# Optimization experiments

Measured on AMD Instinct MI355X. Metric: run time of the kernel, lower is better.

## Reference

```python
import jax, jax.numpy as jnp
import numpy as np

N = 100000   # nodes
E = 1600000  # edges (avg degree 16)
F_IN = 256
H = 64
C = 16


def setup_inputs() -> dict:
    key = jax.random.key(0)
    k1, k2, k3, k4 = jax.random.split(key, 4)
    x = jax.random.normal(k1, (N, F_IN), jnp.float32)
    edge_index = jax.random.randint(k2, (2, E), 0, N, jnp.int32)
    W1 = jax.random.normal(k3, (F_IN, H), jnp.float32) * (1.0 / np.sqrt(F_IN))
    b1 = jnp.zeros((H,), jnp.float32)
    W2 = jax.random.normal(k4, (H, C), jnp.float32) * (1.0 / np.sqrt(H))
    b2 = jnp.zeros((C,), jnp.float32)
    return {"x": x, "edge_index": edge_index, "W1": W1, "b1": b1, "W2": W2, "b2": b2}


def _gcn_conv(h_in, src, dst, norm, W, b):
    # linear transform first (GCNConv: lin has no bias), then normalized scatter-add
    h = h_in @ W                                  # [N, out]
    msg = jnp.take(h, src, axis=0) * norm[:, None]  # [E+N, out] gathered + scaled
    out = jax.ops.segment_sum(msg, dst, num_segments=h_in.shape[0])
    return out + b


def reference(x, edge_index, W1, b1, W2, b2):
    num_nodes = x.shape[0]
    # add self-loops (GCNConv default, edge_weight = 1)
    loop = jnp.arange(num_nodes, dtype=edge_index.dtype)
    src = jnp.concatenate([edge_index[0], loop])
    dst = jnp.concatenate([edge_index[1], loop])
    # symmetric normalization D^{-1/2} A D^{-1/2}
    deg = jax.ops.segment_sum(jnp.ones_like(dst, dtype=x.dtype), dst, num_segments=num_nodes)
    dinv = jnp.where(deg > 0, jax.lax.rsqrt(deg), 0.0)
    norm = jnp.take(dinv, src) * jnp.take(dinv, dst)  # [E+N]
    h = jax.nn.relu(_gcn_conv(x, src, dst, norm, W1, b1))
    # dropout is identity in eval mode
    out = _gcn_conv(h, src, dst, norm, W2, b2)
    return jax.nn.log_softmax(out, axis=1)
```

## Files before the change

kernel.cpp:

```cpp
#include <hip/hip_runtime.h>
#include <hip/hip_fp16.h>
#include <math.h>

#define N_NODES 100000
#define N_EDGES 1600000
#define FIN 256
#define NB 196
#define CAP 10240

typedef _Float16 h8 __attribute__((ext_vector_type(8)));
typedef float f4 __attribute__((ext_vector_type(4)));

__global__ __launch_bounds__(256) void k_prepW1(const float* __restrict__ W1, _Float16* __restrict__ Bfrag) {
    int i = blockIdx.x * 256 + threadIdx.x;
    int j = i & 7, lane = (i >> 3) & 63, nt = (i >> 9) & 3, ks = i >> 11;
    int k = ks * 32 + ((lane >> 4) << 3) + j;
    int c = nt * 16 + (lane & 15);
    Bfrag[i] = (_Float16)W1[k * 64 + c];
}

__global__ __launch_bounds__(256) void k_fill_bins(const int* __restrict__ src, const int* __restrict__ dst,
                                                   int* __restrict__ bcur, int* __restrict__ bpack) {
    __shared__ int hist[NB], curs[NB], bstart[NB];
    const int tid = threadIdx.x;
    for (int i = tid; i < NB; i += 256) { hist[i] = 0; curs[i] = 0; }
    __syncthreads();
    const int base = blockIdx.x * 4096;
    int eb[16], ee[16];
    #pragma unroll
    for (int k = 0; k < 16; ++k) {
        int e = base + k * 256 + tid;
        eb[k] = -1;
        if (e < N_EDGES) {
            int s = src[e], d = dst[e];
            int b = d >> 9;
            eb[k] = b;
            ee[k] = ((d & 511) << 17) | s;
            atomicAdd(&hist[b], 1);
        }
    }
    __syncthreads();
    for (int i = tid; i < NB; i += 256)
        if (hist[i] > 0) bstart[i] = i * CAP + atomicAdd(&bcur[i], hist[i]);
    __syncthreads();
    #pragma unroll
    for (int k = 0; k < 16; ++k) {
        if (eb[k] >= 0) {
            int r = atomicAdd(&curs[eb[k]], 1);
            bpack[bstart[eb[k]] + r] = ee[k];
        }
    }
}

__global__ __launch_bounds__(512) void k_sort_bins(const int* __restrict__ bcur,
                                                   const int* __restrict__ bpack,
                                                   int* __restrict__ pack,
                                                   int* __restrict__ starts,
                                                   int* __restrict__ ends,
                                                   float* __restrict__ dinv) {
    __shared__ int hist[512], sd[512], cur[512];
    const int tid = threadIdx.x;
    const int b = blockIdx.x;
    const int node0 = b << 9;
    hist[tid] = 0;
    __syncthreads();
    const int s0 = b * CAP, s1 = s0 + bcur[b];
    for (int i = s0 + tid; i < s1; i += 512) atomicAdd(&hist[bpack[i] >> 17], 1);
    __syncthreads();
    const int deg = hist[tid];
    sd[tid] = deg;
    __syncthreads();
    for (int off = 1; off < 512; off <<= 1) {
        int tv = (tid >= off) ? sd[tid - off] : 0;
        __syncthreads();
        sd[tid] += tv;
        __syncthreads();
    }
    const int excl = sd[tid] - deg;
    const int n = node0 + tid;
    cur[tid] = s0 + excl;
    if (n < N_NODES) {
        starts[n] = s0 + excl;
        ends[n]   = s0 + excl + deg;
        dinv[n] = rsqrtf((float)deg + 1.0f);
    }
    __syncthreads();
    for (int i = s0 + tid; i < s1; i += 512) {
        int v = bpack[i];
        int pos = atomicAdd(&cur[v >> 17], 1);
        pack[pos] = v & 0x1FFFF;
    }
}

__global__ __launch_bounds__(256) void k_gemm1(const float* __restrict__ x,
                                               const _Float16* __restrict__ Bfrag,
                                               const float* __restrict__ dinv,
                                               __half* __restrict__ hh) {
    const int tid = threadIdx.x;
    const int wave = tid >> 6, lane = tid & 63;
    const int lrow = lane & 15;
    const int lk = lane >> 4;
    const int row = blockIdx.x * 64 + wave * 16 + lrow;
    const int rowc = (row < N_NODES) ? row : (N_NODES - 1);
    const float di = dinv[rowc];
    const float* xp = x + (size_t)rowc * 256 + lk * 8;
    const h8* bp = (const h8*)Bfrag + lane;

    f4 acc0 = {0.f, 0.f, 0.f, 0.f};
    f4 acc1 = {0.f, 0.f, 0.f, 0.f};
    f4 acc2 = {0.f, 0.f, 0.f, 0.f};
    f4 acc3 = {0.f, 0.f, 0.f, 0.f};

    #pragma unroll 2
    for (int ks = 0; ks < 8; ++ks) {
        float4 a01 = *(const float4*)(xp + ks * 32);
        float4 a23 = *(const float4*)(xp + ks * 32 + 4);
        h8 af;
        af[0] = (_Float16)(a01.x * di); af[1] = (_Float16)(a01.y * di);
        af[2] = (_Float16)(a01.z * di); af[3] = (_Float16)(a01.w * di);
        af[4] = (_Float16)(a23.x * di); af[5] = (_Float16)(a23.y * di);
        af[6] = (_Float16)(a23.z * di); af[7] = (_Float16)(a23.w * di);
        h8 b0 = bp[(ks * 4 + 0) * 64];
        h8 b1 = bp[(ks * 4 + 1) * 64];
        h8 b2 = bp[(ks * 4 + 2) * 64];
        h8 b3 = bp[(ks * 4 + 3) * 64];
        acc0 = __builtin_amdgcn_mfma_f32_16x16x32_f16(af, b0, acc0, 0, 0, 0);
        acc1 = __builtin_amdgcn_mfma_f32_16x16x32_f16(af, b1, acc1, 0, 0, 0);
        acc2 = __builtin_amdgcn_mfma_f32_16x16x32_f16(af, b2, acc2, 0, 0, 0);
        acc3 = __builtin_amdgcn_mfma_f32_16x16x32_f16(af, b3, acc3, 0, 0, 0);
    }

    const int orow0 = blockIdx.x * 64 + wave * 16 + lk * 4;
    const bool evlane = ((lane & 1) == 0);
#define STORE_TILE(ACC, NT) { \
    _Pragma("unroll") \
    for (int r = 0; r < 4; ++r) { \
        float v = ACC[r]; \
        float o = __shfl_xor(v, 1); \
        int orow = orow0 + r; \
        if (evlane && orow < N_NODES) \
            *(__half2*)&hh[(size_t)orow * 64 + (NT) * 16 + lrow] = __floats2half2_rn(v, o); \
    } }
    STORE_TILE(acc0, 0)
    STORE_TILE(acc1, 1)
    STORE_TILE(acc2, 2)
    STORE_TILE(acc3, 3)
#undef STORE_TILE
}

__global__ __launch_bounds__(256) void k_agg1_gemm2(const int* __restrict__ starts,
                                                    const int* __restrict__ ends,
                                                    const int* __restrict__ pack,
                                                    const float* __restrict__ dinv,
                                                    const __half* __restrict__ hh,
                                                    const float* __restrict__ b1,
                                                    const float* __restrict__ W2,
                                                    __half* __restrict__ h2h) {
    __shared__ float W2s[64][17];
    __shared__ float h1s[4][64];
    const int tid = threadIdx.x;
    for (int i = tid; i < 64 * 16; i += 256) W2s[i >> 4][i & 15] = W2[i];
    __syncthreads();

    const int wave = tid >> 6;
    const int lane = tid & 63;
    const int node = blockIdx.x * 4 + wave;
    const int e4 = lane >> 4;
    const int l4 = lane & 15;

    const int s0 = starts[node], s1 = ends[node];
    float4 A = {0.f, 0.f, 0.f, 0.f}, B = {0.f, 0.f, 0.f, 0.f};
    int i = s0;
    for (; i + 7 < s1; i += 8) {
        int p0 = pack[i + e4], p1 = pack[i + 4 + e4];
        uint2 r0 = *(const uint2*)(hh + (size_t)p0 * 64 + 4 * l4);
        uint2 r1 = *(const uint2*)(hh + (size_t)p1 * 64 + 4 * l4);
        float2 f00 = __half22float2(*(const __half2*)&r0.x);
        float2 f01 = __half22float2(*(const __half2*)&r0.y);
        float2 f10 = __half22float2(*(const __half2*)&r1.x);
        float2 f11 = __half22float2(*(const __half2*)&r1.y);
        A.x += f00.x; A.y += f00.y; A.z += f01.x; A.w += f01.y;
        B.x += f10.x; B.y += f10.y; B.z += f11.x; B.w += f11.y;
    }
    for (; i + 3 < s1; i += 4) {
        int p = pack[i + e4];
        uint2 r = *(const uint2*)(hh + (size_t)p * 64 + 4 * l4);
        float2 f0 = __half22float2(*(const __half2*)&r.x);
        float2 f1 = __half22float2(*(const __half2*)&r.y);
        A.x += f0.x; A.y += f0.y; A.z += f1.x; A.w += f1.y;
    }
    if (i + e4 < s1) {
        int p = pack[i + e4];
        uint2 r = *(const uint2*)(hh + (size_t)p * 64 + 4 * l4);
        float2 f0 = __half22float2(*(const __half2*)&r.x);
        float2 f1 = __half22float2(*(const __half2*)&r.y);
        A.x += f0.x; A.y += f0.y; A.z += f1.x; A.w += f1.y;
    }
    A.x += B.x; A.y += B.y; A.z += B.z; A.w += B.w;
    A.x += __shfl_xor(A.x, 16); A.y += __shfl_xor(A.y, 16);
    A.z += __shfl_xor(A.z, 16); A.w += __shfl_xor(A.w, 16);
    A.x += __shfl_xor(A.x, 32); A.y += __shfl_xor(A.y, 32);
    A.z += __shfl_xor(A.z, 32); A.w += __shfl_xor(A.w, 32);

    const float di = dinv[node];
    if (lane < 16) {
        uint2 sr = *(const uint2*)(hh + (size_t)node * 64 + 4 * l4);
        float2 sf0 = __half22float2(*(const __half2*)&sr.x);
        float2 sf1 = __half22float2(*(const __half2*)&sr.y);
        h1s[wave][4 * l4 + 0] = fmaxf((A.x + sf0.x) * di + b1[4 * l4 + 0], 0.f);
        h1s[wave][4 * l4 + 1] = fmaxf((A.y + sf0.y) * di + b1[4 * l4 + 1], 0.f);
        h1s[wave][4 * l4 + 2] = fmaxf((A.z + sf1.x) * di + b1[4 * l4 + 2], 0.f);
        h1s[wave][4 * l4 + 3] = fmaxf((A.w + sf1.y) * di + b1[4 * l4 + 3], 0.f);
    }
    const int j = lane >> 4, cc = lane & 15;
    float g = 0.f;
    #pragma unroll
    for (int t = 0; t < 16; ++t) {
        int k = j * 16 + t;
        g = fmaf(h1s[wave][k], W2s[k][cc], g);
    }
    g += __shfl_xor(g, 16);
    g += __shfl_xor(g, 32);
    g *= di;
    float go = __shfl_xor(g, 1);
    if (lane < 16 && (cc & 1) == 0) {
        *(__half2*)&h2h[(size_t)node * 16 + cc] = __floats2half2_rn(g, go);
    }
}

__global__ __launch_bounds__(256) void k_agg2_final(const int* __restrict__ starts,
                                                    const int* __restrict__ ends,
                                                    const int* __restrict__ pack,
                                                    const float* __restrict__ dinv,
                                                    const __half* __restrict__ h2h,
                                                    const float* __restrict__ b2,
                                                    float* __restrict__ out) {
    const int tid = threadIdx.x;
    const int wave = tid >> 6;
    const int lane = tid & 63;
    const int node = blockIdx.x * 4 + wave;
    const int j = lane >> 3, cp = lane & 7;

    const int s0 = starts[node], s1 = ends[node];
    float2 a0 = {0.f, 0.f}, a1 = {0.f, 0.f};
    int i = s0 + j;
    for (; i + 8 < s1; i += 16) {
        int p0 = pack[i], p1 = pack[i + 8];
        float2 f0 = __half22float2(*(const __half2*)(h2h + (size_t)p0 * 16 + 2 * cp));
        float2 f1 = __half22float2(*(const __half2*)(h2h + (size_t)p1 * 16 + 2 * cp));
        a0.x += f0.x; a0.y += f0.y;
        a1.x += f1.x; a1.y += f1.y;
    }
    for (; i < s1; i += 8) {
        int p = pack[i];
        float2 f = __half22float2(*(const __half2*)(h2h + (size_t)p * 16 + 2 * cp));
        a0.x += f.x; a0.y += f.y;
    }
    float2 z;
    z.x = a0.x + a1.x;
    z.y = a0.y + a1.y;
    z.x += __shfl_xor(z.x, 8);  z.y += __shfl_xor(z.y, 8);
    z.x += __shfl_xor(z.x, 16); z.y += __shfl_xor(z.y, 16);
    z.x += __shfl_xor(z.x, 32); z.y += __shfl_xor(z.y, 32);

    const float di = dinv[node];
    float2 sf = __half22float2(*(const __half2*)(h2h + (size_t)node * 16 + 2 * cp));
    z.x = (z.x + sf.x) * di + b2[2 * cp];
    z.y = (z.y + sf.y) * di + b2[2 * cp + 1];

    float m = fmaxf(z.x, z.y);
    m = fmaxf(m, __shfl_xor(m, 1, 8));
    m = fmaxf(m, __shfl_xor(m, 2, 8));
    m = fmaxf(m, __shfl_xor(m, 4, 8));
    float ex = __expf(z.x - m), ey = __expf(z.y - m);
    float s = ex + ey;
    s += __shfl_xor(s, 1, 8);
    s += __shfl_xor(s, 2, 8);
    s += __shfl_xor(s, 4, 8);
    float ls = logf(s);
    if (j == 0) {
        float2 o;
        o.x = z.x - m - ls;
        o.y = z.y - m - ls;
        *(float2*)&out[(size_t)node * 16 + 2 * cp] = o;
    }
}

extern "C" void kernel_launch(void* const* d_in, const int* in_sizes, int n_in,
                              void* d_out, int out_size, void* d_ws, size_t ws_size,
                              hipStream_t stream) {
    const float* x  = (const float*)d_in[0];
    const int* ei   = (const int*)d_in[1];
    const float* W1 = (const float*)d_in[2];
    const float* b1 = (const float*)d_in[3];
    const float* W2 = (const float*)d_in[4];
    const float* b2 = (const float*)d_in[5];
    const int* src = ei;
    const int* dst = ei + N_EDGES;

    _Float16* Bfrag = (_Float16*)d_ws;
    int*    bcur    = (int*)d_ws + 8192;
    int*    starts  = bcur + NB;
    int*    ends    = starts + N_NODES;
    float*  dinv    = (float*)(ends + N_NODES);
    int*    bpack   = (int*)(dinv + N_NODES);
    int*    pack    = bpack + NB * CAP;
    __half* hh      = (__half*)(pack + NB * CAP);
    __half* h2h     = hh + (size_t)N_NODES * 64;
    float*  out     = (float*)d_out;

    hipMemsetAsync(bcur, 0, NB * sizeof(int), stream);

    k_prepW1<<<64, 256, 0, stream>>>(W1, Bfrag);
    k_fill_bins<<<(N_EDGES + 4095) / 4096, 256, 0, stream>>>(src, dst, bcur, bpack);
    k_sort_bins<<<NB, 512, 0, stream>>>(bcur, bpack, pack, starts, ends, dinv);
    k_gemm1<<<(N_NODES + 63) / 64, 256, 0, stream>>>(x, Bfrag, dinv, hh);
    k_agg1_gemm2<<<N_NODES / 4, 256, 0, stream>>>(starts, ends, pack, dinv, hh, b1, W2, h2h);
    k_agg2_final<<<N_NODES / 4, 256, 0, stream>>>(starts, ends, pack, dinv, h2h, b2, out);
}
```

Baseline: 181.5 us.

## Split layer-1 features into column quarters for cache-friendly aggregation, separate GEMM2

The layer-1 transformed features are stored as four column-quarter planes of 16 halves each, so each aggregation pass gathers from a 3.2 MB working set that fits better in cache. Aggregation runs as four interleaved block groups, one per quarter, and processes 16 edges per wave step. The fused aggregation+GEMM2 kernel is split into k_agg1q plus a separate k_gemm2 that reads the intermediate h1 back from memory. The split adds a kernel launch and an extra write and read of the hidden activations, and the neighbor index lists are now read four times.

Result: slower. 224.0 us (+23.4%).

```diff
diff --git a/kernel.cpp b/kernel.cpp
--- a/kernel.cpp
+++ b/kernel.cpp
@@ -139,7 +139,7 @@
         float o = __shfl_xor(v, 1); \
         int orow = orow0 + r; \
         if (evlane && orow < N_NODES) \
-            *(__half2*)&hh[(size_t)orow * 64 + (NT) * 16 + lrow] = __floats2half2_rn(v, o); \
+            *(__half2*)&hh[((size_t)(NT) * N_NODES + orow) * 16 + lrow] = __floats2half2_rn(v, o); \
     } }
     STORE_TILE(acc0, 0)
     STORE_TILE(acc1, 1)
@@ -148,84 +148,99 @@
 #undef STORE_TILE
 }
 
-__global__ __launch_bounds__(256) void k_agg1_gemm2(const int* __restrict__ starts,
-                                                    const int* __restrict__ ends,
-                                                    const int* __restrict__ pack,
-                                                    const float* __restrict__ dinv,
-                                                    const __half* __restrict__ hh,
-                                                    const float* __restrict__ b1,
-                                                    const float* __restrict__ W2,
-                                                    __half* __restrict__ h2h) {
+__global__ __launch_bounds__(256) void k_agg1q(const int* __restrict__ starts,
+                                               const int* __restrict__ ends,
+                                               const int* __restrict__ pack,
+                                               const float* __restrict__ dinv,
+                                               const __half* __restrict__ hh,
+                                               const float* __restrict__ b1,
+                                               __half* __restrict__ h1p) {
+    const int tid = threadIdx.x;
+    const int q = blockIdx.x & 3;
+    const int g = blockIdx.x >> 2;
+    const int wave = tid >> 6, lane = tid & 63;
+    const int e16 = lane >> 2, c4 = lane & 3;
+    const __half* hq = hh + (size_t)q * N_NODES * 16;
+
+    for (int nn = 0; nn < 4; ++nn) {
+        const int node = g * 16 + wave * 4 + nn;
+        const int s0 = starts[node], s1 = ends[node];
+        float4 A = {0.f, 0.f, 0.f, 0.f}, Bv = {0.f, 0.f, 0.f, 0.f};
+        int i = s0;
+        for (; i + 31 < s1; i += 32) {
+            int p0 = pack[i + e16], p1 = pack[i + 16 + e16];
+            uint2 r0 = *(const uint2*)(hq + (size_t)p0 * 16 + c4 * 4);
+            uint2 r1 = *(const uint2*)(hq + (size_t)p1 * 16 + c4 * 4);
+            float2 f00 = __half22float2(*(const __half2*)&r0.x);
+            float2 f01 = __half22float2(*(const __half2*)&r0.y);
+            float2 f10 = __half22float2(*(const __half2*)&r1.x);
+            float2 f11 = __half22float2(*(const __half2*)&r1.y);
+            A.x += f00.x; A.y += f00.y; A.z += f01.x; A.w += f01.y;
+            Bv.x += f10.x; Bv.y += f10.y; Bv.z += f11.x; Bv.w += f11.y;
+        }
+        for (; i < s1; i += 16) {
+            if (i + e16 < s1) {
+                int p = pack[i + e16];
+                uint2 r = *(const uint2*)(hq + (size_t)p * 16 + c4 * 4);
+                float2 f0 = __half22float2(*(const __half2*)&r.x);
+                float2 f1 = __half22float2(*(const __half2*)&r.y);
+                A.x += f0.x; A.y += f0.y; A.z += f1.x; A.w += f1.y;
+            }
+        }
+        A.x += Bv.x; A.y += Bv.y; A.z += Bv.z; A.w += Bv.w;
+        A.x += __shfl_xor(A.x, 4);  A.y += __shfl_xor(A.y, 4);
+        A.z += __shfl_xor(A.z, 4);  A.w += __shfl_xor(A.w, 4);
+        A.x += __shfl_xor(A.x, 8);  A.y += __shfl_xor(A.y, 8);
+        A.z += __shfl_xor(A.z, 8);  A.w += __shfl_xor(A.w, 8);
+        A.x += __shfl_xor(A.x, 16); A.y += __shfl_xor(A.y, 16);
+        A.z += __shfl_xor(A.z, 16); A.w += __shfl_xor(A.w, 16);
+        A.x += __shfl_xor(A.x, 32); A.y += __shfl_xor(A.y, 32);
+        A.z += __shfl_xor(A.z, 32); A.w += __shfl_xor(A.w, 32);
+        if (lane < 4) {
+            const float di = dinv[node];
+            uint2 sr = *(const uint2*)(hq + (size_t)node * 16 + c4 * 4);
+            float2 sf0 = __half22float2(*(const __half2*)&sr.x);
+            float2 sf1 = __half22float2(*(const __half2*)&sr.y);
+            const float* bq = b1 + q * 16 + c4 * 4;
+            float v0 = fmaxf((A.x + sf0.x) * di + bq[0], 0.f);
+            float v1 = fmaxf((A.y + sf0.y) * di + bq[1], 0.f);
+            float v2 = fmaxf((A.z + sf1.x) * di + bq[2], 0.f);
+            float v3 = fmaxf((A.w + sf1.y) * di + bq[3], 0.f);
+            __half2 o0 = __floats2half2_rn(v0, v1);
+            __half2 o1 = __floats2half2_rn(v2, v3);
+            uint2 ov = { *(unsigned*)&o0, *(unsigned*)&o1 };
+            *(uint2*)(h1p + ((size_t)q * N_NODES + node) * 16 + c4 * 4) = ov;
+        }
+    }
+}
+
+__global__ __launch_bounds__(256) void k_gemm2(const __half* __restrict__ h1p,
+                                               const float* __restrict__ dinv,
+                                               const float* __restrict__ W2,
+                                               __half* __restrict__ h2h) {
     __shared__ float W2s[64][17];
-    __shared__ float h1s[4][64];
+    __shared__ float h1s[16][65];
     const int tid = threadIdx.x;
     for (int i = tid; i < 64 * 16; i += 256) W2s[i >> 4][i & 15] = W2[i];
-    __syncthreads();
-
-    const int wave = tid >> 6;
-    const int lane = tid & 63;
-    const int node = blockIdx.x * 4 + wave;
-    const int e4 = lane >> 4;
-    const int l4 = lane & 15;
-
-    const int s0 = starts[node], s1 = ends[node];
-    float4 A = {0.f, 0.f, 0.f, 0.f}, B = {0.f, 0.f, 0.f, 0.f};
-    int i = s0;
-    for (; i + 7 < s1; i += 8) {
-        int p0 = pack[i + e4], p1 = pack[i + 4 + e4];
-        uint2 r0 = *(const uint2*)(hh + (size_t)p0 * 64 + 4 * l4);
-        uint2 r1 = *(const uint2*)(hh + (size_t)p1 * 64 + 4 * l4);
-        float2 f00 = __half22float2(*(const __half2*)&r0.x);
-        float2 f01 = __half22float2(*(const __half2*)&r0.y);
-        float2 f10 = __half22float2(*(const __half2*)&r1.x);
-        float2 f11 = __half22float2(*(const __half2*)&r1.y);
-        A.x += f00.x; A.y += f00.y; A.z += f01.x; A.w += f01.y;
-        B.x += f10.x; B.y += f10.y; B.z += f11.x; B.w += f11.y;
-    }
-    for (; i + 3 < s1; i += 4) {
-        int p = pack[i + e4];
-        uint2 r = *(const uint2*)(hh + (size_t)p * 64 + 4 * l4);
+    const int node0 = blockIdx.x * 16;
+    {
+        int n = tid >> 4, c0 = (tid & 15) * 4;
+        int q = c0 >> 4, cin = c0 & 15;
+        uint2 r = *(const uint2*)(h1p + ((size_t)q * N_NODES + node0 + n) * 16 + cin);
         float2 f0 = __half22float2(*(const __half2*)&r.x);
         float2 f1 = __half22float2(*(const __half2*)&r.y);
-        A.x += f0.x; A.y += f0.y; A.z += f1.x; A.w += f1.y;
-    }
-    if (i + e4 < s1) {
-        int p = pack[i + e4];
-        uint2 r = *(const uint2*)(hh + (size_t)p * 64 + 4 * l4);
-        float2 f0 = __half22float2(*(const __half2*)&r.x);
-        float2 f1 = __half22float2(*(const __half2*)&r.y);
-        A.x += f0.x; A.y += f0.y; A.z += f1.x; A.w += f1.y;
-    }
-    A.x += B.x; A.y += B.y; A.z += B.z; A.w += B.w;
-    A.x += __shfl_xor(A.x, 16); A.y += __shfl_xor(A.y, 16);
-    A.z += __shfl_xor(A.z, 16); A.w += __shfl_xor(A.w, 16);
-    A.x += __shfl_xor(A.x, 32); A.y += __shfl_xor(A.y, 32);
-    A.z += __shfl_xor(A.z, 32); A.w += __shfl_xor(A.w, 32);
-
-    const float di = dinv[node];
-    if (lane < 16) {
-        uint2 sr = *(const uint2*)(hh + (size_t)node * 64 + 4 * l4);
-        float2 sf0 = __half22float2(*(const __half2*)&sr.x);
-        float2 sf1 = __half22float2(*(const __half2*)&sr.y);
-        h1s[wave][4 * l4 + 0] = fmaxf((A.x + sf0.x) * di + b1[4 * l4 + 0], 0.f);
-        h1s[wave][4 * l4 + 1] = fmaxf((A.y + sf0.y) * di + b1[4 * l4 + 1], 0.f);
-        h1s[wave][4 * l4 + 2] = fmaxf((A.z + sf1.x) * di + b1[4 * l4 + 2], 0.f);
-        h1s[wave][4 * l4 + 3] = fmaxf((A.w + sf1.y) * di + b1[4 * l4 + 3], 0.f);
-    }
-    const int j = lane >> 4, cc = lane & 15;
+        h1s[n][c0 + 0] = f0.x; h1s[n][c0 + 1] = f0.y;
+        h1s[n][c0 + 2] = f1.x; h1s[n][c0 + 3] = f1.y;
+    }
+    __syncthreads();
+    const int n = tid >> 4, c = tid & 15;
     float g = 0.f;
     #pragma unroll
-    for (int t = 0; t < 16; ++t) {
-        int k = j * 16 + t;
-        g = fmaf(h1s[wave][k], W2s[k][cc], g);
-    }
-    g += __shfl_xor(g, 16);
-    g += __shfl_xor(g, 32);
-    g *= di;
+    for (int k = 0; k < 64; ++k) g = fmaf(h1s[n][k], W2s[k][c], g);
+    g *= dinv[node0 + n];
     float go = __shfl_xor(g, 1);
-    if (lane < 16 && (cc & 1) == 0) {
-        *(__half2*)&h2h[(size_t)node * 16 + cc] = __floats2half2_rn(g, go);
-    }
+    if ((c & 1) == 0)
+        *(__half2*)&h2h[(size_t)(node0 + n) * 16 + c] = __floats2half2_rn(g, go);
 }
 
 __global__ __launch_bounds__(256) void k_agg2_final(const int* __restrict__ starts,
@@ -306,7 +321,8 @@
     int*    bpack   = (int*)(dinv + N_NODES);
     int*    pack    = bpack + NB * CAP;
     __half* hh      = (__half*)(pack + NB * CAP);
-    __half* h2h     = hh + (size_t)N_NODES * 64;
+    __half* h1p     = hh + (size_t)N_NODES * 64;
+    __half* h2h     = h1p + (size_t)N_NODES * 64;
     float*  out     = (float*)d_out;
 
     hipMemsetAsync(bcur, 0, NB * sizeof(int), stream);
@@ -315,6 +331,7 @@
     k_fill_bins<<<(N_EDGES + 4095) / 4096, 256, 0, stream>>>(src, dst, bcur, bpack);
     k_sort_bins<<<NB, 512, 0, stream>>>(bcur, bpack, pack, starts, ends, dinv);
     k_gemm1<<<(N_NODES + 63) / 64, 256, 0, stream>>>(x, Bfrag, dinv, hh);
-    k_agg1_gemm2<<<N_NODES / 4, 256, 0, stream>>>(starts, ends, pack, dinv, hh, b1, W2, h2h);
+    k_agg1q<<<(N_NODES / 16) * 4, 256, 0, stream>>>(starts, ends, pack, dinv, hh, b1, h1p);
+    k_gemm2<<<N_NODES / 16, 256, 0, stream>>>(h1p, dinv, W2, h2h);
     k_agg2_final<<<N_NODES / 4, 256, 0, stream>>>(starts, ends, pack, dinv, h2h, b2, out);
 }
```
